# Kernel tuning notes

Hardware: AMD Instinct MI355X
Metric: run time of the kernel (lower is better)

Reference implementation:

```python
import jax, jax.numpy as jnp
import numpy as np

N = 100000
E = 500000
D = 128      # input_dim
H = 4        # heads
C = 32       # per-head out channels (H*C == D)
HID = 512    # FFN hidden
EPS = 1e-5


def _layer_norm(x, w, b):
    mu = jnp.mean(x, axis=-1, keepdims=True)
    var = jnp.mean(jnp.square(x - mu), axis=-1, keepdims=True)
    return (x - mu) * jax.lax.rsqrt(var + EPS) * w + b


def setup_inputs() -> dict:
    key = jax.random.key(0)
    ks = jax.random.split(key, 16)
    s = 1.0 / np.sqrt(D)
    inp = {
        "x": jax.random.normal(ks[0], (N, D), dtype=jnp.float32),
        "edge_index": jax.random.randint(ks[1], (2, E), 0, N, dtype=jnp.int64),
        # TransformerConv params (lin_query/key/value/skip: D -> H*C == D)
        "Wq": jax.random.normal(ks[2], (D, D), dtype=jnp.float32) * s,
        "bq": jnp.zeros((D,), jnp.float32),
        "Wk": jax.random.normal(ks[3], (D, D), dtype=jnp.float32) * s,
        "bk": jnp.zeros((D,), jnp.float32),
        "Wv": jax.random.normal(ks[4], (D, D), dtype=jnp.float32) * s,
        "bv": jnp.zeros((D,), jnp.float32),
        "Wskip": jax.random.normal(ks[5], (D, D), dtype=jnp.float32) * s,
        "bskip": jnp.zeros((D,), jnp.float32),
        # lin_out
        "Wout": jax.random.normal(ks[6], (D, D), dtype=jnp.float32) * s,
        "bout": jnp.zeros((D,), jnp.float32),
        # LayerNorms
        "ln1_w": jnp.ones((D,), jnp.float32),
        "ln1_b": jnp.zeros((D,), jnp.float32),
        "ln2_w": jnp.ones((D,), jnp.float32),
        "ln2_b": jnp.zeros((D,), jnp.float32),
        # FFN
        "W1": jax.random.normal(ks[7], (HID, D), dtype=jnp.float32) * s,
        "b1": jnp.zeros((HID,), jnp.float32),
        "W2": jax.random.normal(ks[8], (D, HID), dtype=jnp.float32) * (1.0 / np.sqrt(HID)),
        "b2": jnp.zeros((D,), jnp.float32),
    }
    return inp


def _transformer_conv(x, src, dst, Wq, bq, Wk, bk, Wv, bv, Wskip, bskip):
    # q/k/v: [N, H, C]
    q = (x @ Wq.T + bq).reshape(N, H, C)
    k = (x @ Wk.T + bk).reshape(N, H, C)
    v = (x @ Wv.T + bv).reshape(N, H, C)
    # per-edge attention logits: [E, H]
    alpha = jnp.sum(q[dst] * k[src], axis=-1) / np.sqrt(C)
    # segment softmax over incoming edges of each destination node
    m = jax.ops.segment_max(alpha, dst, num_segments=N)       # [N, H]
    e = jnp.exp(alpha - m[dst])                               # [E, H]
    z = jax.ops.segment_sum(e, dst, num_segments=N)           # [N, H]
    a = e / z[dst]                                            # [E, H]
    # weighted aggregate of values: [N, H, C]
    msg = a[:, :, None] * v[src]
    out = jax.ops.segment_sum(msg, dst, num_segments=N)
    # root/skip connection (PyG root_weight=True)
    return out.reshape(N, H * C) + x @ Wskip.T + bskip


def reference(x, Wq, bq, Wk, bk, Wv, bv, Wskip, bskip, Wout, bout,
              ln1_w, ln1_b, W1, b1, W2, b2, ln2_w, ln2_b, edge_index):
    src = edge_index[0]
    dst = edge_index[1]
    conv = _transformer_conv(x, src, dst, Wq, bq, Wk, bk, Wv, bv, Wskip, bskip)
    out1 = conv @ Wout.T + bout
    out2 = _layer_norm(out1 + x, ln1_w, ln1_b)
    h = jax.nn.relu(out2 @ W1.T + b1)
    out3 = h @ W2.T + b2
    out4 = _layer_norm(out3 + out2, ln2_w, ln2_b)
    return out4
```

## Files before the change

kernel.cpp:

```cpp
#include <hip/hip_runtime.h>

#define NN   100000
#define NE   500000
#define DD   128
#define HH   4
#define HIDD 512
#define EPSF 1e-5f

typedef __bf16 bf16x8 __attribute__((ext_vector_type(8)));
typedef float  f32x4  __attribute__((ext_vector_type(4)));

__device__ __forceinline__ unsigned short f2b(float f) {
  unsigned u = __float_as_uint(f);
  unsigned r = (u + 0x7FFFu + ((u >> 16) & 1)) >> 16;
  return (unsigned short)r;
}
__device__ __forceinline__ float b2f(unsigned short s) {
  return __uint_as_float(((unsigned)s) << 16);
}

#define GLOAD16(ldsp, gp) __builtin_amdgcn_global_load_lds(                      \
    (const __attribute__((address_space(1))) void*)(gp),                         \
    (__attribute__((address_space(3))) void*)(ldsp), 16, 0, 0)

__device__ __forceinline__ void stageW(unsigned short* lds, const unsigned short* g,
                                       int ldg, int t) {
  const int w = t >> 6, l = t & 63;
#pragma unroll
  for (int i = 0; i < 8; i++) {
    const int chunk0 = i * 256 + w * 64;
    const int chunk = chunk0 + l;
    const int row = chunk >> 4, c16 = chunk & 15;
    const int gslot = c16 ^ (row & 15);
    GLOAD16(lds + (size_t)chunk0 * 8, g + (size_t)row * ldg + gslot * 8);
  }
}

__global__ void k_cast(const float* __restrict__ src, unsigned short* __restrict__ dst, int n) {
  int i = (blockIdx.x * 256 + threadIdx.x) * 4;
  if (i >= n) return;
  float4 v = *(const float4*)&src[i];
  ushort4 o;
  o.x = f2b(v.x); o.y = f2b(v.y); o.z = f2b(v.z); o.w = f2b(v.w);
  *(ushort4*)&dst[i] = o;
}

__global__ void k_castw(const float* __restrict__ Wq, const float* __restrict__ Wk,
                        const float* __restrict__ Wv, const float* __restrict__ Wsk,
                        const float* __restrict__ Wo, const float* __restrict__ W1,
                        const float* __restrict__ W2,
                        const float* __restrict__ bq, const float* __restrict__ bk,
                        const float* __restrict__ bv, const float* __restrict__ bs,
                        unsigned short* __restrict__ Wqkvs, unsigned short* __restrict__ Wob,
                        unsigned short* __restrict__ W1b, unsigned short* __restrict__ W2b,
                        float* __restrict__ bias512) {
  int i = blockIdx.x * 256 + threadIdx.x;
  if (i < 53248) {
    int e = i * 4;
    const float* src; unsigned short* dst; int off;
    if (e < 65536) {
      int seg = e >> 14;
      const float* s4[4] = {Wq, Wk, Wv, Wsk};
      src = s4[seg]; dst = Wqkvs + (seg << 14); off = e & 16383;
    } else if (e < 81920) { src = Wo;  dst = Wob; off = e - 65536; }
    else if (e < 147456)  { src = W1;  dst = W1b; off = e - 81920; }
    else                  { src = W2;  dst = W2b; off = e - 147456; }
    float4 v = *(const float4*)&src[off];
    ushort4 o; o.x = f2b(v.x); o.y = f2b(v.y); o.z = f2b(v.z); o.w = f2b(v.w);
    *(ushort4*)&dst[off] = o;
  } else if (i < 53376) {
    int b4 = (i - 53248) * 4;
    const float* srcs[4] = {bq, bk, bv, bs};
#pragma unroll
    for (int j = 0; j < 4; j++) {
      int idx = b4 + j;
      bias512[idx] = srcs[idx >> 7][idx & 127];
    }
  }
}

__global__ void k_zero_cnt(int* __restrict__ cnt) {
  int i = blockIdx.x * 256 + threadIdx.x;
  if (i < NN) cnt[i] = 0;
}
__global__ void k_count(const int* __restrict__ ei, int* __restrict__ cnt) {
  int e = blockIdx.x * 256 + threadIdx.x;
  if (e < NE) atomicAdd(&cnt[ei[NE + e]], 1);
}
__global__ void k_scan1(const int* __restrict__ cnt, int* __restrict__ rowptr, int* __restrict__ part) {
  __shared__ int sh[256];
  int i = blockIdx.x * 256 + threadIdx.x;
  int v = (i < NN) ? cnt[i] : 0;
  sh[threadIdx.x] = v; __syncthreads();
  for (int off = 1; off < 256; off <<= 1) {
    int t = (threadIdx.x >= off) ? sh[threadIdx.x - off] : 0;
    __syncthreads();
    sh[threadIdx.x] += t;
    __syncthreads();
  }
  if (i < NN) rowptr[i] = sh[threadIdx.x] - v;
  if (threadIdx.x == 255) part[blockIdx.x] = sh[255];
}
__global__ void k_scan2(const int* __restrict__ part, int* __restrict__ partx) {
  __shared__ int sh[512];
  int t = threadIdx.x;
  int v = (t < 391) ? part[t] : 0;
  sh[t] = v; __syncthreads();
  for (int off = 1; off < 512; off <<= 1) {
    int u = (t >= off) ? sh[t - off] : 0;
    __syncthreads();
    sh[t] += u;
    __syncthreads();
  }
  partx[t] = sh[t] - v;
}
__global__ void k_scan3(int* __restrict__ rowptr, const int* __restrict__ partx, int* __restrict__ cnt) {
  int i = blockIdx.x * 256 + threadIdx.x;
  if (i < NN) {
    int r = rowptr[i] + partx[i >> 8];
    rowptr[i] = r;
    cnt[i] = r;
  }
  if (i == 0) rowptr[NN] = NE;
}
__global__ void k_scatter(const int* __restrict__ ei, int* __restrict__ cnt, int* __restrict__ csr_src) {
  int e = blockIdx.x * 256 + threadIdx.x;
  if (e >= NE) return;
  int d = ei[NE + e];
  int pos = atomicAdd(&cnt[d], 1);
  csr_src[pos] = ei[e];
}

template <int KTOT, int LDA, bool RELU, int MODE, int MW>
__global__ __launch_bounds__(256, MW) void k_gemm_wl(const unsigned short* __restrict__ A,
                                                     const unsigned short* __restrict__ W,
                                                     const float* __restrict__ bias,
                                                     const unsigned short* __restrict__ resB,
                                                     const float* __restrict__ lw,
                                                     const float* __restrict__ lb,
                                                     float* __restrict__ outF,
                                                     unsigned short* __restrict__ outB) {
  __shared__ __align__(16) unsigned short Ws[128 * 128];
  const int t = threadIdx.x;
  const int w = t >> 6, l = t & 63;
  const int bx   = (MODE == 0) ? (blockIdx.x >> 2) : blockIdx.x;
  const int col0 = (MODE == 0) ? (blockIdx.x & 3) * 128 : 0;
  const int n0 = bx * 128 + w * 32;
  const int lq = l & 15, hq = l >> 4;

#define LOADA2(dst, kb)                                                          \
  _Pragma("unroll") for (int ks = 0; ks < 4; ks++)                               \
    _Pragma("unroll") for (int rt = 0; rt < 2; rt++) {                           \
      const int row_ = n0 + rt * 16 + lq;                                        \
      bf16x8 zz = {};                                                            \
      dst[ks][rt] = (row_ < NN)                                                  \
          ? *(const bf16x8*)&A[(size_t)row_ * LDA + (kb) + ks * 32 + hq * 8]     \
          : zz;                                                                  \
    }

  f32x4 acc[2][8] = {};
  bf16x8 afr[4][2];
  LOADA2(afr, 0);
  stageW(Ws, W + (size_t)col0 * KTOT, KTOT, t);
  __syncthreads();
  constexpr int NC = KTOT / 128;
#pragma unroll
  for (int kc = 0; kc < NC; ++kc) {
    bf16x8 anx[4][2];
    if (kc + 1 < NC) LOADA2(anx, (kc + 1) * 128);
#pragma unroll
    for (int ks = 0; ks < 4; ks++) {
      bf16x8 b[8];
      const int c16 = ks * 4 + hq;
#pragma unroll
      for (int ct = 0; ct < 8; ct++) {
        const int row = ct * 16 + lq;
        b[ct] = *(const bf16x8*)&Ws[row * 128 + ((c16 ^ lq) * 8)];
      }
#pragma unroll
      for (int rt = 0; rt < 2; rt++)
#pragma unroll
        for (int ct = 0; ct < 8; ct++)
          acc[rt][ct] = __builtin_amdgcn_mfma_f32_16x16x32_bf16(b[ct], afr[ks][rt], acc[rt][ct], 0, 0, 0);
    }
    if (kc + 1 < NC) {
      __syncthreads();
      stageW(Ws, W + (size_t)col0 * KTOT + (kc + 1) * 128, KTOT, t);
      __syncthreads();
#pragma unroll
      for (int ks = 0; ks < 4; ks++)
#pragma unroll
        for (int rt = 0; rt < 2; rt++) afr[ks][rt] = anx[ks][rt];
    }
  }

  if constexpr (MODE == 0) {
#pragma unroll
    for (int rt = 0; rt < 2; rt++) {
      const int row = n0 + rt * 16 + lq;
      if (row < NN) {
#pragma unroll
        for (int ct = 0; ct < 8; ct++) {
          const int col = col0 + ct * 16 + hq * 4;
          const float4 bs = *(const float4*)&bias[col];
          float v0 = acc[rt][ct][0] + bs.x, v1 = acc[rt][ct][1] + bs.y;
          float v2 = acc[rt][ct][2] + bs.z, v3 = acc[rt][ct][3] + bs.w;
          if (RELU) {
            v0 = fmaxf(v0, 0.f); v1 = fmaxf(v1, 0.f);
            v2 = fmaxf(v2, 0.f); v3 = fmaxf(v3, 0.f);
          }
          ushort4 o; o.x = f2b(v0); o.y = f2b(v1); o.z = f2b(v2); o.w = f2b(v3);
          *(ushort4*)&outB[(size_t)row * 512 + col] = o;
        }
      }
    }
  } else {
#pragma unroll
    for (int rt = 0; rt < 2; rt++) {
      const int row = n0 + rt * 16 + lq;
#pragma unroll
      for (int ct = 0; ct < 8; ct++) {
        const int col = ct * 16 + hq * 4;
        const float4 bs = *(const float4*)&bias[col];
        ushort4 rv = make_ushort4(0, 0, 0, 0);
        if (row < NN) rv = *(const ushort4*)&resB[(size_t)row * DD + col];
        acc[rt][ct][0] += bs.x + b2f(rv.x);
        acc[rt][ct][1] += bs.y + b2f(rv.y);
        acc[rt][ct][2] += bs.z + b2f(rv.z);
        acc[rt][ct][3] += bs.w + b2f(rv.w);
      }
      float s = 0.f;
#pragma unroll
      for (int ct = 0; ct < 8; ct++)
#pragma unroll
        for (int j = 0; j < 4; j++) s += acc[rt][ct][j];
      s += __shfl_xor(s, 16, 64); s += __shfl_xor(s, 32, 64);
      const float mu = s * (1.f / 128.f);
      float vs = 0.f;
#pragma unroll
      for (int ct = 0; ct < 8; ct++)
#pragma unroll
        for (int j = 0; j < 4; j++) { float d = acc[rt][ct][j] - mu; vs += d * d; }
      vs += __shfl_xor(vs, 16, 64); vs += __shfl_xor(vs, 32, 64);
      const float rs = rsqrtf(vs * (1.f / 128.f) + EPSF);
      if (row < NN) {
#pragma unroll
        for (int ct = 0; ct < 8; ct++) {
          const int col = ct * 16 + hq * 4;
          const float4 lw4 = *(const float4*)&lw[col];
          const float4 lb4 = *(const float4*)&lb[col];
          float y0 = (acc[rt][ct][0] - mu) * rs * lw4.x + lb4.x;
          float y1 = (acc[rt][ct][1] - mu) * rs * lw4.y + lb4.y;
          float y2 = (acc[rt][ct][2] - mu) * rs * lw4.z + lb4.z;
          float y3 = (acc[rt][ct][3] - mu) * rs * lw4.w + lb4.w;
          if (MODE == 2) {
            float4 o; o.x = y0; o.y = y1; o.z = y2; o.w = y3;
            *(float4*)&outF[(size_t)row * DD + col] = o;
          } else {
            ushort4 o; o.x = f2b(y0); o.y = f2b(y1); o.z = f2b(y2); o.w = f2b(y3);
            *(ushort4*)&outB[(size_t)row * DD + col] = o;
          }
        }
      }
    }
  }
#undef LOADA2
}

__global__ __launch_bounds__(256) void k_attn(const int* __restrict__ csr_src,
                                              const int* __restrict__ rowptr,
                                              unsigned short* qkvsb) {
  const int l = threadIdx.x & 31;
  const int node = blockIdx.x * 8 + (threadIdx.x >> 5);
  const int row0 = rowptr[node], row1 = rowptr[node + 1];
  ushort4 qu = *(const ushort4*)&qkvsb[(size_t)node * 512 + l * 4];
  const float qx = b2f(qu.x), qy = b2f(qu.y), qz = b2f(qu.z), qw = b2f(qu.w);
  float ax = 0.f, ay = 0.f, az = 0.f, aw = 0.f, z = 0.f;
  int p = row0;
  for (; p + 2 <= row1; p += 2) {
    int s0 = csr_src[p], s1 = csr_src[p + 1];
    const unsigned short* b0 = &qkvsb[(size_t)s0 * 512];
    const unsigned short* b1 = &qkvsb[(size_t)s1 * 512];
    ushort4 k0 = *(const ushort4*)(b0 + 128 + l * 4);
    ushort4 v0 = *(const ushort4*)(b0 + 256 + l * 4);
    ushort4 k1 = *(const ushort4*)(b1 + 128 + l * 4);
    ushort4 v1 = *(const ushort4*)(b1 + 256 + l * 4);
    float d0 = qx * b2f(k0.x) + qy * b2f(k0.y) + qz * b2f(k0.z) + qw * b2f(k0.w);
    float d1 = qx * b2f(k1.x) + qy * b2f(k1.y) + qz * b2f(k1.z) + qw * b2f(k1.w);
    d0 += __shfl_xor(d0, 1, 32); d1 += __shfl_xor(d1, 1, 32);
    d0 += __shfl_xor(d0, 2, 32); d1 += __shfl_xor(d1, 2, 32);
    d0 += __shfl_xor(d0, 4, 32); d1 += __shfl_xor(d1, 4, 32);
    float e0 = __expf(d0 * 0.17677669529663687f);
    float e1 = __expf(d1 * 0.17677669529663687f);
    z += e0 + e1;
    ax += e0 * b2f(v0.x) + e1 * b2f(v1.x);
    ay += e0 * b2f(v0.y) + e1 * b2f(v1.y);
    az += e0 * b2f(v0.z) + e1 * b2f(v1.z);
    aw += e0 * b2f(v0.w) + e1 * b2f(v1.w);
  }
  if (p < row1) {
    int s = csr_src[p];
    const unsigned short* base = &qkvsb[(size_t)s * 512];
    ushort4 kr = *(const ushort4*)(base + 128 + l * 4);
    ushort4 vr = *(const ushort4*)(base + 256 + l * 4);
    float d = qx * b2f(kr.x) + qy * b2f(kr.y) + qz * b2f(kr.z) + qw * b2f(kr.w);
    d += __shfl_xor(d, 1, 32);
    d += __shfl_xor(d, 2, 32);
    d += __shfl_xor(d, 4, 32);
    float e = __expf(d * 0.17677669529663687f);
    z += e;
    ax += e * b2f(vr.x); ay += e * b2f(vr.y);
    az += e * b2f(vr.z); aw += e * b2f(vr.w);
  }
  const float rz = (z > 0.f) ? (1.f / z) : 0.f;
  ushort4 su = *(const ushort4*)&qkvsb[(size_t)node * 512 + 384 + l * 4];
  ushort4 o;
  o.x = f2b(b2f(su.x) + ax * rz);
  o.y = f2b(b2f(su.y) + ay * rz);
  o.z = f2b(b2f(su.z) + az * rz);
  o.w = f2b(b2f(su.w) + aw * rz);
  *(ushort4*)&qkvsb[(size_t)node * 512 + 384 + l * 4] = o;
}

extern "C" void kernel_launch(void* const* d_in, const int* in_sizes, int n_in,
                              void* d_out, int out_size, void* d_ws, size_t ws_size,
                              hipStream_t stream) {
  const float* x   = (const float*)d_in[0];
  const int*   ei  = (const int*)d_in[1];
  const float* Wq  = (const float*)d_in[2];
  const float* bq  = (const float*)d_in[3];
  const float* Wk  = (const float*)d_in[4];
  const float* bk  = (const float*)d_in[5];
  const float* Wv  = (const float*)d_in[6];
  const float* bv  = (const float*)d_in[7];
  const float* Wsk = (const float*)d_in[8];
  const float* bsk = (const float*)d_in[9];
  const float* Wo  = (const float*)d_in[10];
  const float* bo  = (const float*)d_in[11];
  const float* l1w = (const float*)d_in[12];
  const float* l1b = (const float*)d_in[13];
  const float* l2w = (const float*)d_in[14];
  const float* l2b = (const float*)d_in[15];
  const float* W1  = (const float*)d_in[16];
  const float* b1  = (const float*)d_in[17];
  const float* W2  = (const float*)d_in[18];
  const float* b2  = (const float*)d_in[19];

  unsigned short* wsu = (unsigned short*)d_ws;
  unsigned short* qkvsb = wsu;
  unsigned short* out2b = wsu + (size_t)NN * 512;
  unsigned short* xb    = out2b + (size_t)NN * DD;
  int* csr_src = (int*)(xb + (size_t)NN * DD);
  int* rowptr  = csr_src + NE;
  int* cnt     = rowptr + NN + 1;
  int* part    = cnt + NN;
  int* partx   = part + 512;
  size_t woff = (size_t)((partx + 512) - (int*)d_ws);
  woff = (woff + 3) & ~(size_t)3;
  unsigned short* Wqkvs = (unsigned short*)((int*)d_ws + woff);
  unsigned short* Wob   = Wqkvs + 512 * DD;
  unsigned short* W1b   = Wob + DD * DD;
  unsigned short* W2b   = W1b + (size_t)HIDD * DD;
  float* bias512        = (float*)(W2b + (size_t)DD * HIDD);

  unsigned short* hid = qkvsb;
  float* outf = (float*)d_out;

  const int GX = (NN + 127) / 128;
  dim3 blk(256);

  k_cast<<<dim3(12500), blk, 0, stream>>>(x, xb, NN * DD);
  k_castw<<<dim3(209), blk, 0, stream>>>(Wq, Wk, Wv, Wsk, Wo, W1, W2, bq, bk, bv, bsk,
                                         Wqkvs, Wob, W1b, W2b, bias512);

  k_zero_cnt<<<dim3(391), blk, 0, stream>>>(cnt);
  k_count<<<dim3(1954), blk, 0, stream>>>(ei, cnt);
  k_scan1<<<dim3(391), blk, 0, stream>>>(cnt, rowptr, part);
  k_scan2<<<dim3(1), dim3(512), 0, stream>>>(part, partx);
  k_scan3<<<dim3(391), blk, 0, stream>>>(rowptr, partx, cnt);
  k_scatter<<<dim3(1954), blk, 0, stream>>>(ei, cnt, csr_src);

  k_gemm_wl<128, 128, false, 0, 4><<<dim3(GX * 4), blk, 0, stream>>>(
      xb, Wqkvs, bias512, nullptr, nullptr, nullptr, nullptr, qkvsb);

  k_attn<<<dim3(12500), blk, 0, stream>>>(csr_src, rowptr, qkvsb);

  k_gemm_wl<128, 512, false, 1, 4><<<dim3(GX), blk, 0, stream>>>(
      qkvsb + 384, Wob, bo, xb, l1w, l1b, nullptr, out2b);

  k_gemm_wl<128, 128, true, 0, 4><<<dim3(GX * 4), blk, 0, stream>>>(
      out2b, W1b, b1, nullptr, nullptr, nullptr, nullptr, hid);

  k_gemm_wl<512, 512, false, 2, 3><<<dim3(GX), blk, 0, stream>>>(
      hid, W2b, b2, out2b, l2w, l2b, outf, nullptr);
}
```

Baseline: 325.3 us.

## Fuse FFN up/down GEMMs through LDS and loop column groups in QKV GEMM

```diff
diff --git a/kernel.cpp b/kernel.cpp
--- a/kernel.cpp
+++ b/kernel.cpp
@@ -131,43 +131,173 @@
   csr_src[pos] = ei[e];
 }
 
-template <int KTOT, int LDA, bool RELU, int MODE, int MW>
-__global__ __launch_bounds__(256, MW) void k_gemm_wl(const unsigned short* __restrict__ A,
+#define LOADA(dst, Aptr, LDA_, kb)                                               \
+  _Pragma("unroll") for (int ks = 0; ks < 4; ks++)                               \
+    _Pragma("unroll") for (int rt = 0; rt < 2; rt++) {                           \
+      const int row_ = n0 + rt * 16 + lq;                                        \
+      bf16x8 zz = {};                                                            \
+      dst[ks][rt] = (row_ < NN)                                                  \
+          ? *(const bf16x8*)&(Aptr)[(size_t)row_ * (LDA_) + (kb) + ks * 32 + hq * 8] \
+          : zz;                                                                  \
+    }
+
+__global__ __launch_bounds__(256, 2) void k_gemm_cg(const unsigned short* __restrict__ A,
+                                                    const unsigned short* __restrict__ W,
+                                                    const float* __restrict__ bias,
+                                                    unsigned short* __restrict__ outB) {
+  __shared__ __align__(16) unsigned short Ws[128 * 128];
+  const int t = threadIdx.x;
+  const int w = t >> 6, l = t & 63;
+  const int n0 = blockIdx.x * 128 + w * 32;
+  const int lq = l & 15, hq = l >> 4;
+
+  bf16x8 af[4][2];
+  LOADA(af, A, 128, 0);
+#pragma unroll 1
+  for (int cg = 0; cg < 4; ++cg) {
+    if (cg) __syncthreads();
+    stageW(Ws, W + (size_t)cg * 128 * 128, 128, t);
+    __syncthreads();
+    f32x4 acc[2][8] = {};
+#pragma unroll
+    for (int ks = 0; ks < 4; ks++) {
+      bf16x8 b[8];
+      const int c16 = ks * 4 + hq;
+#pragma unroll
+      for (int ct = 0; ct < 8; ct++) {
+        const int row = ct * 16 + lq;
+        b[ct] = *(const bf16x8*)&Ws[row * 128 + ((c16 ^ lq) * 8)];
+      }
+#pragma unroll
+      for (int rt = 0; rt < 2; rt++)
+#pragma unroll
+        for (int ct = 0; ct < 8; ct++)
+          acc[rt][ct] = __builtin_amdgcn_mfma_f32_16x16x32_bf16(b[ct], af[ks][rt], acc[rt][ct], 0, 0, 0);
+    }
+#pragma unroll
+    for (int rt = 0; rt < 2; rt++) {
+      const int row = n0 + rt * 16 + lq;
+      if (row < NN) {
+#pragma unroll
+        for (int ct = 0; ct < 8; ct++) {
+          const int col = cg * 128 + ct * 16 + hq * 4;
+          const float4 bs = *(const float4*)&bias[col];
+          ushort4 o;
+          o.x = f2b(acc[rt][ct][0] + bs.x);
+          o.y = f2b(acc[rt][ct][1] + bs.y);
+          o.z = f2b(acc[rt][ct][2] + bs.z);
+          o.w = f2b(acc[rt][ct][3] + bs.w);
+          *(ushort4*)&outB[(size_t)row * 512 + col] = o;
+        }
+      }
+    }
+  }
+}
+
+__global__ __launch_bounds__(256, 4) void k_gemm_ln1(const unsigned short* __restrict__ A,
                                                      const unsigned short* __restrict__ W,
                                                      const float* __restrict__ bias,
                                                      const unsigned short* __restrict__ resB,
                                                      const float* __restrict__ lw,
                                                      const float* __restrict__ lb,
-                                                     float* __restrict__ outF,
                                                      unsigned short* __restrict__ outB) {
   __shared__ __align__(16) unsigned short Ws[128 * 128];
   const int t = threadIdx.x;
   const int w = t >> 6, l = t & 63;
-  const int bx   = (MODE == 0) ? (blockIdx.x >> 2) : blockIdx.x;
-  const int col0 = (MODE == 0) ? (blockIdx.x & 3) * 128 : 0;
-  const int n0 = bx * 128 + w * 32;
+  const int n0 = blockIdx.x * 128 + w * 32;
   const int lq = l & 15, hq = l >> 4;
 
-#define LOADA2(dst, kb)                                                          \
-  _Pragma("unroll") for (int ks = 0; ks < 4; ks++)                               \
-    _Pragma("unroll") for (int rt = 0; rt < 2; rt++) {                           \
-      const int row_ = n0 + rt * 16 + lq;                                        \
-      bf16x8 zz = {};                                                            \
-      dst[ks][rt] = (row_ < NN)                                                  \
-          ? *(const bf16x8*)&A[(size_t)row_ * LDA + (kb) + ks * 32 + hq * 8]     \
-          : zz;                                                                  \
-    }
-
+  bf16x8 af[4][2];
+  LOADA(af, A, 512, 0);
+  stageW(Ws, W, 128, t);
+  __syncthreads();
   f32x4 acc[2][8] = {};
-  bf16x8 afr[4][2];
-  LOADA2(afr, 0);
-  stageW(Ws, W + (size_t)col0 * KTOT, KTOT, t);
-  __syncthreads();
-  constexpr int NC = KTOT / 128;
-#pragma unroll
-  for (int kc = 0; kc < NC; ++kc) {
-    bf16x8 anx[4][2];
-    if (kc + 1 < NC) LOADA2(anx, (kc + 1) * 128);
+#pragma unroll
+  for (int ks = 0; ks < 4; ks++) {
+    bf16x8 b[8];
+    const int c16 = ks * 4 + hq;
+#pragma unroll
+    for (int ct = 0; ct < 8; ct++) {
+      const int row = ct * 16 + lq;
+      b[ct] = *(const bf16x8*)&Ws[row * 128 + ((c16 ^ lq) * 8)];
+    }
+#pragma unroll
+    for (int rt = 0; rt < 2; rt++)
+#pragma unroll
+      for (int ct = 0; ct < 8; ct++)
+        acc[rt][ct] = __builtin_amdgcn_mfma_f32_16x16x32_bf16(b[ct], af[ks][rt], acc[rt][ct], 0, 0, 0);
+  }
+#pragma unroll
+  for (int rt = 0; rt < 2; rt++) {
+    const int row = n0 + rt * 16 + lq;
+#pragma unroll
+    for (int ct = 0; ct < 8; ct++) {
+      const int col = ct * 16 + hq * 4;
+      const float4 bs = *(const float4*)&bias[col];
+      ushort4 rv = make_ushort4(0, 0, 0, 0);
+      if (row < NN) rv = *(const ushort4*)&resB[(size_t)row * DD + col];
+      acc[rt][ct][0] += bs.x + b2f(rv.x);
+      acc[rt][ct][1] += bs.y + b2f(rv.y);
+      acc[rt][ct][2] += bs.z + b2f(rv.z);
+      acc[rt][ct][3] += bs.w + b2f(rv.w);
+    }
+    float s = 0.f;
+#pragma unroll
+    for (int ct = 0; ct < 8; ct++)
+#pragma unroll
+      for (int j = 0; j < 4; j++) s += acc[rt][ct][j];
+    s += __shfl_xor(s, 16, 64); s += __shfl_xor(s, 32, 64);
+    const float mu = s * (1.f / 128.f);
+    float vs = 0.f;
+#pragma unroll
+    for (int ct = 0; ct < 8; ct++)
+#pragma unroll
+      for (int j = 0; j < 4; j++) { float d = acc[rt][ct][j] - mu; vs += d * d; }
+    vs += __shfl_xor(vs, 16, 64); vs += __shfl_xor(vs, 32, 64);
+    const float rs = rsqrtf(vs * (1.f / 128.f) + EPSF);
+    if (row < NN) {
+#pragma unroll
+      for (int ct = 0; ct < 8; ct++) {
+        const int col = ct * 16 + hq * 4;
+        const float4 lw4 = *(const float4*)&lw[col];
+        const float4 lb4 = *(const float4*)&lb[col];
+        ushort4 o;
+        o.x = f2b((acc[rt][ct][0] - mu) * rs * lw4.x + lb4.x);
+        o.y = f2b((acc[rt][ct][1] - mu) * rs * lw4.y + lb4.y);
+        o.z = f2b((acc[rt][ct][2] - mu) * rs * lw4.z + lb4.z);
+        o.w = f2b((acc[rt][ct][3] - mu) * rs * lw4.w + lb4.w);
+        *(ushort4*)&outB[(size_t)row * DD + col] = o;
+      }
+    }
+  }
+}
+
+__global__ __launch_bounds__(256, 2) void k_ffn_fused(const unsigned short* __restrict__ A,
+                                                      const unsigned short* __restrict__ W1,
+                                                      const float* __restrict__ b1,
+                                                      const unsigned short* __restrict__ W2,
+                                                      const float* __restrict__ b2,
+                                                      const float* __restrict__ lw,
+                                                      const float* __restrict__ lb,
+                                                      float* __restrict__ outF) {
+  __shared__ __align__(16) unsigned short Ws[128 * 128];
+  __shared__ __align__(16) unsigned short Hs[128 * 128];
+  const int t = threadIdx.x;
+  const int w = t >> 6, l = t & 63;
+  const int n0 = blockIdx.x * 128 + w * 32;
+  const int lq = l & 15, hq = l >> 4;
+  const int lrow = w * 32;
+
+  bf16x8 af[4][2];
+  LOADA(af, A, 128, 0);
+
+  f32x4 acc2[2][8] = {};
+#pragma unroll 1
+  for (int cg = 0; cg < 4; ++cg) {
+    if (cg) __syncthreads();
+    stageW(Ws, W1 + (size_t)cg * 128 * 128, 128, t);
+    __syncthreads();
+    f32x4 acc1[2][8] = {};
 #pragma unroll
     for (int ks = 0; ks < 4; ks++) {
       bf16x8 b[8];
@@ -181,90 +311,92 @@
       for (int rt = 0; rt < 2; rt++)
 #pragma unroll
         for (int ct = 0; ct < 8; ct++)
-          acc[rt][ct] = __builtin_amdgcn_mfma_f32_16x16x32_bf16(b[ct], afr[ks][rt], acc[rt][ct], 0, 0, 0);
-    }
-    if (kc + 1 < NC) {
-      __syncthreads();
-      stageW(Ws, W + (size_t)col0 * KTOT + (kc + 1) * 128, KTOT, t);
-      __syncthreads();
-#pragma unroll
-      for (int ks = 0; ks < 4; ks++)
-#pragma unroll
-        for (int rt = 0; rt < 2; rt++) afr[ks][rt] = anx[ks][rt];
-    }
-  }
-
-  if constexpr (MODE == 0) {
+          acc1[rt][ct] = __builtin_amdgcn_mfma_f32_16x16x32_bf16(b[ct], af[ks][rt], acc1[rt][ct], 0, 0, 0);
+    }
 #pragma unroll
     for (int rt = 0; rt < 2; rt++) {
-      const int row = n0 + rt * 16 + lq;
-      if (row < NN) {
-#pragma unroll
-        for (int ct = 0; ct < 8; ct++) {
-          const int col = col0 + ct * 16 + hq * 4;
-          const float4 bs = *(const float4*)&bias[col];
-          float v0 = acc[rt][ct][0] + bs.x, v1 = acc[rt][ct][1] + bs.y;
-          float v2 = acc[rt][ct][2] + bs.z, v3 = acc[rt][ct][3] + bs.w;
-          if (RELU) {
-            v0 = fmaxf(v0, 0.f); v1 = fmaxf(v1, 0.f);
-            v2 = fmaxf(v2, 0.f); v3 = fmaxf(v3, 0.f);
-          }
-          ushort4 o; o.x = f2b(v0); o.y = f2b(v1); o.z = f2b(v2); o.w = f2b(v3);
-          *(ushort4*)&outB[(size_t)row * 512 + col] = o;
-        }
-      }
-    }
-  } else {
-#pragma unroll
-    for (int rt = 0; rt < 2; rt++) {
-      const int row = n0 + rt * 16 + lq;
+      const int row = lrow + rt * 16 + lq;
 #pragma unroll
       for (int ct = 0; ct < 8; ct++) {
         const int col = ct * 16 + hq * 4;
-        const float4 bs = *(const float4*)&bias[col];
-        ushort4 rv = make_ushort4(0, 0, 0, 0);
-        if (row < NN) rv = *(const ushort4*)&resB[(size_t)row * DD + col];
-        acc[rt][ct][0] += bs.x + b2f(rv.x);
-        acc[rt][ct][1] += bs.y + b2f(rv.y);
-        acc[rt][ct][2] += bs.z + b2f(rv.z);
-        acc[rt][ct][3] += bs.w + b2f(rv.w);
-      }
-      float s = 0.f;
-#pragma unroll
-      for (int ct = 0; ct < 8; ct++)
-#pragma unroll
-        for (int j = 0; j < 4; j++) s += acc[rt][ct][j];
-      s += __shfl_xor(s, 16, 64); s += __shfl_xor(s, 32, 64);
-      const float mu = s * (1.f / 128.f);
-      float vs = 0.f;
-#pragma unroll
-      for (int ct = 0; ct < 8; ct++)
-#pragma unroll
-        for (int j = 0; j < 4; j++) { float d = acc[rt][ct][j] - mu; vs += d * d; }
-      vs += __shfl_xor(vs, 16, 64); vs += __shfl_xor(vs, 32, 64);
-      const float rs = rsqrtf(vs * (1.f / 128.f) + EPSF);
-      if (row < NN) {
-#pragma unroll
-        for (int ct = 0; ct < 8; ct++) {
-          const int col = ct * 16 + hq * 4;
-          const float4 lw4 = *(const float4*)&lw[col];
-          const float4 lb4 = *(const float4*)&lb[col];
-          float y0 = (acc[rt][ct][0] - mu) * rs * lw4.x + lb4.x;
-          float y1 = (acc[rt][ct][1] - mu) * rs * lw4.y + lb4.y;
-          float y2 = (acc[rt][ct][2] - mu) * rs * lw4.z + lb4.z;
-          float y3 = (acc[rt][ct][3] - mu) * rs * lw4.w + lb4.w;
-          if (MODE == 2) {
-            float4 o; o.x = y0; o.y = y1; o.z = y2; o.w = y3;
-            *(float4*)&outF[(size_t)row * DD + col] = o;
-          } else {
-            ushort4 o; o.x = f2b(y0); o.y = f2b(y1); o.z = f2b(y2); o.w = f2b(y3);
-            *(ushort4*)&outB[(size_t)row * DD + col] = o;
-          }
-        }
-      }
-    }
-  }
-#undef LOADA2
+        const float4 bs = *(const float4*)&b1[cg * 128 + col];
+        ushort4 o;
+        o.x = f2b(fmaxf(acc1[rt][ct][0] + bs.x, 0.f));
+        o.y = f2b(fmaxf(acc1[rt][ct][1] + bs.y, 0.f));
+        o.z = f2b(fmaxf(acc1[rt][ct][2] + bs.z, 0.f));
+        o.w = f2b(fmaxf(acc1[rt][ct][3] + bs.w, 0.f));
+        *(ushort4*)&Hs[row * 128 + (((col >> 3) ^ lq) * 8) + (col & 7)] = o;
+      }
+    }
+    __syncthreads();
+    stageW(Ws, W2 + (size_t)cg * 128, 512, t);
+    __syncthreads();
+#pragma unroll
+    for (int ks = 0; ks < 4; ks++) {
+      bf16x8 b[8];
+      const int c16 = ks * 4 + hq;
+#pragma unroll
+      for (int ct = 0; ct < 8; ct++) {
+        const int row = ct * 16 + lq;
+        b[ct] = *(const bf16x8*)&Ws[row * 128 + ((c16 ^ lq) * 8)];
+      }
+      bf16x8 h[2];
+#pragma unroll
+      for (int rt = 0; rt < 2; rt++) {
+        const int row = lrow + rt * 16 + lq;
+        h[rt] = *(const bf16x8*)&Hs[row * 128 + (((ks * 4 + hq) ^ lq) * 8)];
+      }
+#pragma unroll
+      for (int rt = 0; rt < 2; rt++)
+#pragma unroll
+        for (int ct = 0; ct < 8; ct++)
+          acc2[rt][ct] = __builtin_amdgcn_mfma_f32_16x16x32_bf16(b[ct], h[rt], acc2[rt][ct], 0, 0, 0);
+    }
+  }
+
+#pragma unroll
+  for (int rt = 0; rt < 2; rt++) {
+    const int row = n0 + rt * 16 + lq;
+#pragma unroll
+    for (int ct = 0; ct < 8; ct++) {
+      const int col = ct * 16 + hq * 4;
+      const float4 bs = *(const float4*)&b2[col];
+      ushort4 rv = make_ushort4(0, 0, 0, 0);
+      if (row < NN) rv = *(const ushort4*)&A[(size_t)row * DD + col];
+      acc2[rt][ct][0] += bs.x + b2f(rv.x);
+      acc2[rt][ct][1] += bs.y + b2f(rv.y);
+      acc2[rt][ct][2] += bs.z + b2f(rv.z);
+      acc2[rt][ct][3] += bs.w + b2f(rv.w);
+    }
+    float s = 0.f;
+#pragma unroll
+    for (int ct = 0; ct < 8; ct++)
+#pragma unroll
+      for (int j = 0; j < 4; j++) s += acc2[rt][ct][j];
+    s += __shfl_xor(s, 16, 64); s += __shfl_xor(s, 32, 64);
+    const float mu = s * (1.f / 128.f);
+    float vs = 0.f;
+#pragma unroll
+    for (int ct = 0; ct < 8; ct++)
+#pragma unroll
+      for (int j = 0; j < 4; j++) { float d = acc2[rt][ct][j] - mu; vs += d * d; }
+    vs += __shfl_xor(vs, 16, 64); vs += __shfl_xor(vs, 32, 64);
+    const float rs = rsqrtf(vs * (1.f / 128.f) + EPSF);
+    if (row < NN) {
+#pragma unroll
+      for (int ct = 0; ct < 8; ct++) {
+        const int col = ct * 16 + hq * 4;
+        const float4 lw4 = *(const float4*)&lw[col];
+        const float4 lb4 = *(const float4*)&lb[col];
+        float4 o;
+        o.x = (acc2[rt][ct][0] - mu) * rs * lw4.x + lb4.x;
+        o.y = (acc2[rt][ct][1] - mu) * rs * lw4.y + lb4.y;
+        o.z = (acc2[rt][ct][2] - mu) * rs * lw4.z + lb4.z;
+        o.w = (acc2[rt][ct][3] - mu) * rs * lw4.w + lb4.w;
+        *(float4*)&outF[(size_t)row * DD + col] = o;
+      }
+    }
+  }
 }
 
 __global__ __launch_bounds__(256) void k_attn(const int* __restrict__ csr_src,
@@ -363,7 +495,6 @@
   unsigned short* W2b   = W1b + (size_t)HIDD * DD;
   float* bias512        = (float*)(W2b + (size_t)DD * HIDD);
 
-  unsigned short* hid = qkvsb;
   float* outf = (float*)d_out;
 
   const int GX = (NN + 127) / 128;
@@ -380,17 +511,11 @@
   k_scan3<<<dim3(391), blk, 0, stream>>>(rowptr, partx, cnt);
   k_scatter<<<dim3(1954), blk, 0, stream>>>(ei, cnt, csr_src);
 
-  k_gemm_wl<128, 128, false, 0, 4><<<dim3(GX * 4), blk, 0, stream>>>(
-      xb, Wqkvs, bias512, nullptr, nullptr, nullptr, nullptr, qkvsb);
+  k_gemm_cg<<<dim3(GX), blk, 0, stream>>>(xb, Wqkvs, bias512, qkvsb);
 
   k_attn<<<dim3(12500), blk, 0, stream>>>(csr_src, rowptr, qkvsb);
 
-  k_gemm_wl<128, 512, false, 1, 4><<<dim3(GX), blk, 0, stream>>>(
-      qkvsb + 384, Wob, bo, xb, l1w, l1b, nullptr, out2b);
-
-  k_gemm_wl<128, 128, true, 0, 4><<<dim3(GX * 4), blk, 0, stream>>>(
-      out2b, W1b, b1, nullptr, nullptr, nullptr, nullptr, hid);
-
-  k_gemm_wl<512, 512, false, 2, 3><<<dim3(GX), blk, 0, stream>>>(
-      hid, W2b, b2, out2b, l2w, l2b, outf, nullptr);
-}
+  k_gemm_ln1<<<dim3(GX), blk, 0, stream>>>(qkvsb + 384, Wob, bo, xb, l1w, l1b, out2b);
+
+  k_ffn_fused<<<dim3(GX), blk, 0, stream>>>(out2b, W1b, b1, W2b, b2, l2w, l2b, outf);
+}
```

New measurement: 271.7 us. -16.5%, faster.
